# Kernel optimization log

Hardware: AMD Instinct MI355X
Metric: run time of the kernel (lower is better)

## Reference

```python
import jax, jax.numpy as jnp
import numpy as np

PAD = 9  # FNO2d self.padding


def conv1x1(x, w, b):
    # x: [B,Ci,H,W], w: [Co,Ci], b: [Co]  (1x1 Conv2d)
    return jnp.einsum('bixy,oi->boxy', x, w) + b[None, :, None, None]


def setup_inputs() -> dict:
    key = jax.random.key(0)
    ks = jax.random.split(key, 16)
    B, S = 16, 128
    Cin, W, M, D = 5, 64, 16, 4  # raw input channels, width, modes, depth
    scale = 1.0 / (W * W)
    f32 = jnp.float32
    inp = {}
    inp['x'] = jax.random.normal(ks[0], (B, Cin, S, S), dtype=f32)
    # lifting Linear p: in_channel=Cin+2 (grid appended) -> width
    inp['p_w'] = 0.1 * jax.random.normal(ks[1], (Cin + 2, W), dtype=f32)
    inp['p_b'] = jnp.zeros((W,), dtype=f32)
    # spectral weights, stored as real/imag pairs: [D,2,Ci,Co,M,M]
    inp['sw1'] = scale * jax.random.uniform(ks[2], (D, 2, W, W, M, M), dtype=f32)
    inp['sw2'] = scale * jax.random.uniform(ks[3], (D, 2, W, W, M, M), dtype=f32)
    # per-layer MLP (two 1x1 convs) and skip 1x1 conv w
    inp['mlp1_w'] = 0.05 * jax.random.normal(ks[4], (D, W, W), dtype=f32)
    inp['mlp1_b'] = jnp.zeros((D, W), dtype=f32)
    inp['mlp2_w'] = 0.05 * jax.random.normal(ks[5], (D, W, W), dtype=f32)
    inp['mlp2_b'] = jnp.zeros((D, W), dtype=f32)
    inp['ww'] = 0.05 * jax.random.normal(ks[6], (D, W, W), dtype=f32)
    inp['wb'] = jnp.zeros((D, W), dtype=f32)
    # projection MLP q: width -> 4*width -> 1
    inp['q1_w'] = 0.05 * jax.random.normal(ks[7], (4 * W, W), dtype=f32)
    inp['q1_b'] = jnp.zeros((4 * W,), dtype=f32)
    inp['q2_w'] = 0.05 * jax.random.normal(ks[8], (1, 4 * W), dtype=f32)
    inp['q2_b'] = jnp.zeros((1,), dtype=f32)
    return inp


def reference(x, p_w, p_b, sw1, sw2, mlp1_w, mlp1_b, mlp2_w, mlp2_b, ww, wb, q1_w, q1_b, q2_w, q2_b):
    B, _, Sx, Sy = x.shape
    D, _, _, Co, M, _ = sw1.shape
    # grid channels (x, y) in [0,1]
    gx = jnp.broadcast_to(jnp.linspace(0.0, 1.0, Sx, dtype=x.dtype)[None, None, :, None], (B, 1, Sx, Sy))
    gy = jnp.broadcast_to(jnp.linspace(0.0, 1.0, Sy, dtype=x.dtype)[None, None, None, :], (B, 1, Sx, Sy))
    x = jnp.concatenate([x, gx, gy], axis=1)
    # lifting (Linear over channel dim)
    x = jnp.einsum('bcxy,cd->bdxy', x, p_w) + p_b[None, :, None, None]
    # pad bottom/right
    x = jnp.pad(x, ((0, 0), (0, 0), (0, PAD), (0, PAD)))
    H, Wd = x.shape[-2], x.shape[-1]
    for i in range(D):
        # spectral conv: rfft2 -> low-mode complex mult -> irfft2
        xf = jnp.fft.rfft2(x)  # [B,C,H,Wd//2+1] complex64
        w1 = sw1[i, 0] + 1j * sw1[i, 1]
        w2 = sw2[i, 0] + 1j * sw2[i, 1]
        top = jnp.einsum('bixy,ioxy->boxy', xf[:, :, :M, :M], w1)
        bot = jnp.einsum('bixy,ioxy->boxy', xf[:, :, H - M:, :M], w2)
        of = jnp.zeros((B, Co, H, Wd // 2 + 1), dtype=xf.dtype)
        of = of.at[:, :, :M, :M].set(top).at[:, :, H - M:, :M].set(bot)
        x1 = jnp.fft.irfft2(of, s=(H, Wd))
        # MLP on spectral branch
        x1 = conv1x1(x1, mlp1_w[i], mlp1_b[i])
        x1 = jax.nn.gelu(x1, approximate=False)
        x1 = conv1x1(x1, mlp2_w[i], mlp2_b[i])
        # skip 1x1 conv
        x2 = conv1x1(x, ww[i], wb[i])
        x = jax.nn.gelu(x1 + x2, approximate=False)
    # crop padding, project
    x = x[..., :H - PAD, :Wd - PAD]
    x = conv1x1(x, q1_w, q1_b)
    x = jax.nn.gelu(x, approximate=False)
    x = conv1x1(x, q2_w, q2_b)
    return x
```

## Files before the change

### kernel.cpp

```cpp
#include <hip/hip_runtime.h>
#include <math.h>

#define BB 16
#define CH 64
#define SS 128
#define HH 137
#define XS 144
#define CS (137 * 144)
#define MM 16
#define KK 32
#define NL 4

__device__ __forceinline__ float gelu_f(float x) {
    return 0.5f * x * (1.0f + erff(x * 0.70710678118654752440f));
}

__global__ void k_init(float2* __restrict__ Wy, float2* __restrict__ Wx,
                       float2* __restrict__ WyT, float* __restrict__ wcomb,
                       const float* __restrict__ m2w, const float* __restrict__ wwp) {
    int t = blockIdx.x * 256 + threadIdx.x;
    const double PI2 = 6.283185307179586476925286766559;
    if (t < 2192) {
        int y = t >> 4, k = t & 15;
        int m = (y * k) % HH;
        double ang = -PI2 * (double)m / (double)HH;
        Wy[t] = make_float2((float)cos(ang), (float)sin(ang));
    } else if (t < 6576) {
        int u = t - 2192;
        int x = u >> 5, ki = u & 31;
        int K = (ki < 16) ? ki : (105 + ki);
        int m = (x * K) % HH;
        double ang = -PI2 * (double)m / (double)HH;
        Wx[u] = make_float2((float)cos(ang), (float)sin(ang));
    } else if (t < 8768) {
        int u = t - 6576;
        int ky = u / 137, y = u - ky * 137;
        int m = (y * ky) % HH;
        double ang = -PI2 * (double)m / (double)HH;
        WyT[u] = make_float2((float)cos(ang), (float)sin(ang));
    } else if (t < 41536) {
        int u = t - 8768;
        int layer = u >> 13;
        int r = u & 8191;
        int i = r >> 7, c = r & 127;
        float v;
        if (c < 64) v = m2w[layer * 4096 + c * 64 + i];
        else        v = wwp[layer * 4096 + (c - 64) * 64 + i];
        wcomb[u] = v;
    }
}

__global__ void k_wtrans(const float* __restrict__ sw1, const float* __restrict__ sw2,
                         int layer, float* __restrict__ WS) {
    int d = blockIdx.x * 256 + threadIdx.x;
    int reim = d & 1;
    int o  = (d >> 1) & 63;
    int i  = (d >> 7) & 63;
    int ky = (d >> 13) & 15;
    int kx = (d >> 17) & 31;
    const float* src = (kx < 16) ? sw1 : sw2;
    int kk = kx & 15;
    WS[d] = src[layer * 2097152 + reim * 1048576 + i * 16384 + o * 256 + kk * 16 + ky];
}

__global__ void k_proj(const float* __restrict__ x, const float* __restrict__ pw,
                       const float* __restrict__ pb, float* __restrict__ X0) {
    int t = blockIdx.x * 256 + threadIdx.x;
    int b = t / (CH * CS);
    int r = t - b * (CH * CS);
    int d = r / CS;
    int s = r - d * CS;
    int X = s / XS, Y = s - X * XS;
    float v = 0.f;
    if (X < SS && Y < SS) {
        v = pb[d];
        #pragma unroll
        for (int c = 0; c < 5; c++)
            v += x[((b * 5 + c) * SS + X) * SS + Y] * pw[c * CH + d];
        v += ((float)X * (1.0f / 127.0f)) * pw[5 * CH + d];
        v += ((float)Y * (1.0f / 127.0f)) * pw[6 * CH + d];
    }
    X0[t] = v;
}

__global__ void __launch_bounds__(256) k_dfty3(const float* __restrict__ X0,
                                               const float2* __restrict__ Wy,
                                               float* __restrict__ Tf) {
    __shared__ float sXT[32 * 260];
    __shared__ float sWy[HH * 32];
    int tid = threadIdx.x;
    int r0b = blockIdx.x * 256;
    int bi0 = r0b / 137;
    int xx0 = r0b - bi0 * 137;
    for (int idx = tid; idx < HH * MM; idx += 256) {
        float2 w = Wy[idx];
        sWy[idx * 2] = w.x;
        sWy[idx * 2 + 1] = w.y;
    }
    int rowg = tid >> 2, kg = tid & 3;
    int r0 = rowg * 4, k0 = kg * 8;
    float acc[4][8];
    #pragma unroll
    for (int a = 0; a < 4; a++)
        #pragma unroll
        for (int c = 0; c < 8; c++) acc[a][c] = 0.f;
    for (int yc = 0; yc < 5; yc++) {
        int y0c = yc * 32;
        int ylen = (y0c + 32 <= HH) ? 32 : (HH - y0c);
        __syncthreads();
        for (int k = 0; k < 8; k++) {
            int idx = k * 256 + tid;
            int r = idx >> 3, q = idx & 7;
            int xx = xx0 + r, bi = bi0;
            if (xx >= 137) { xx -= 137; bi++; }
            if (xx >= 137) { xx -= 137; bi++; }
            int y = y0c + 4 * q;
            size_t off = (size_t)bi * CS + xx * XS + y;
            float4 v;
            if (y + 4 <= HH) {
                v = *(const float4*)&X0[off];
            } else {
                v.x = (y     < HH) ? X0[off]     : 0.f;
                v.y = (y + 1 < HH) ? X0[off + 1] : 0.f;
                v.z = (y + 2 < HH) ? X0[off + 2] : 0.f;
                v.w = (y + 3 < HH) ? X0[off + 3] : 0.f;
            }
            int yy = 4 * q;
            sXT[(yy    ) * 260 + r] = v.x;
            sXT[(yy + 1) * 260 + r] = v.y;
            sXT[(yy + 2) * 260 + r] = v.z;
            sXT[(yy + 3) * 260 + r] = v.w;
        }
        __syncthreads();
        for (int yy = 0; yy < ylen; yy++) {
            int y = y0c + yy;
            float4 wA = *(const float4*)&sWy[y * 32 + k0];
            float4 wB = *(const float4*)&sWy[y * 32 + k0 + 4];
            float4 v  = *(const float4*)&sXT[yy * 260 + r0];
            float wv[8] = {wA.x, wA.y, wA.z, wA.w, wB.x, wB.y, wB.z, wB.w};
            float vv[4] = {v.x, v.y, v.z, v.w};
            #pragma unroll
            for (int a = 0; a < 4; a++)
                #pragma unroll
                for (int c = 0; c < 8; c++) acc[a][c] += vv[a] * wv[c];
        }
    }
    #pragma unroll
    for (int a = 0; a < 4; a++) {
        size_t rb = (size_t)(r0b + r0 + a) * 32 + k0;
        *(float4*)&Tf[rb]     = make_float4(acc[a][0], acc[a][1], acc[a][2], acc[a][3]);
        *(float4*)&Tf[rb + 4] = make_float4(acc[a][4], acc[a][5], acc[a][6], acc[a][7]);
    }
}

__global__ void __launch_bounds__(512) k_dftx2(const float* __restrict__ Tf,
                                               const float2* __restrict__ Wx,
                                               float2* __restrict__ F) {
    __shared__ float sT[HH * 32];
    __shared__ float2 sWx[HH * 32];
    int tid = threadIdx.x;
    int bi = blockIdx.x;
    const float4* tg = (const float4*)(Tf + (size_t)bi * (HH * 32));
    for (int idx = tid; idx < HH * 8; idx += 512) ((float4*)sT)[idx] = tg[idx];
    const float4* wg = (const float4*)Wx;
    for (int idx = tid; idx < HH * 16; idx += 512) ((float4*)sWx)[idx] = wg[idx];
    __syncthreads();
    int ky = tid & 15, kx = tid >> 4;
    float fr = 0.f, fi = 0.f;
    const float2* sT2 = (const float2*)sT;
    #pragma unroll 4
    for (int x = 0; x < HH; x++) {
        float2 t = sT2[x * 16 + ky];
        float2 w = sWx[x * 32 + kx];
        fr += t.x * w.x - t.y * w.y;
        fi += t.x * w.y + t.y * w.x;
    }
    F[(size_t)bi * 512 + tid] = make_float2(fr, fi);
}

__global__ void __launch_bounds__(256) k_specmul2(const float2* __restrict__ F,
                                                  const float2* __restrict__ WS,
                                                  float2* __restrict__ G) {
    int tid = threadIdx.x;
    int o = tid & 63;
    int kyq = __builtin_amdgcn_readfirstlane(tid >> 6);
    int kx = blockIdx.x;
    int bg = blockIdx.y;
    for (int bq = 0; bq < 2; bq++) {
        int b = bg * 2 + bq;
        float gr[4], gi[4];
        #pragma unroll
        for (int j = 0; j < 4; j++) { gr[j] = 0.f; gi[j] = 0.f; }
        for (int i = 0; i < CH; i++) {
            const float2* Fb = F + ((size_t)(b * CH + i) * KK + kx) * MM + kyq * 4;
            const float2* Wb = WS + ((size_t)(kx * MM + kyq * 4) * CH + i) * CH + o;
            #pragma unroll
            for (int j = 0; j < 4; j++) {
                float2 f = Fb[j];
                float2 w = Wb[(size_t)j * CH * CH];
                gr[j] += f.x * w.x - f.y * w.y;
                gi[j] += f.x * w.y + f.y * w.x;
            }
        }
        float* Gf = (float*)G;
        size_t base = (((size_t)(b * CH + o) * KK + kx) * MM + kyq * 4) * 2;
        *(float4*)&Gf[base]     = make_float4(gr[0], gi[0], gr[1], gi[1]);
        *(float4*)&Gf[base + 4] = make_float4(gr[2], gi[2], gr[3], gi[3]);
    }
}

__global__ void __launch_bounds__(128) k_mlp1m(const float* __restrict__ Gf,
                                               const float* __restrict__ m1w, int layer,
                                               float* __restrict__ G2f) {
    __shared__ float sG[64 * 64];
    __shared__ float sM[64 * 68];
    int tid = threadIdx.x;
    int b = blockIdx.y;
    int c0b = blockIdx.x * 64;
    for (int idx = tid; idx < 4096; idx += 128) {
        int o = idx >> 6, c = idx & 63;
        sG[idx] = Gf[(size_t)(b * CH + o) * 1024 + c0b + c];
    }
    for (int idx = tid; idx < 4096; idx += 128) {
        int p = idx >> 6, o = idx & 63;
        sM[o * 68 + p] = m1w[layer * 4096 + p * 64 + o];
    }
    __syncthreads();
    int cg = tid & 15, pg = tid >> 4;
    int c0 = cg * 4, p0 = pg * 8;
    float acc[8][4];
    #pragma unroll
    for (int a = 0; a < 8; a++)
        #pragma unroll
        for (int c = 0; c < 4; c++) acc[a][c] = 0.f;
    for (int o = 0; o < CH; o++) {
        float4 wA = *(const float4*)&sM[o * 68 + p0];
        float4 wB = *(const float4*)&sM[o * 68 + p0 + 4];
        float4 v  = *(const float4*)&sG[o * 64 + c0];
        float wv[8] = {wA.x, wA.y, wA.z, wA.w, wB.x, wB.y, wB.z, wB.w};
        float vv[4] = {v.x, v.y, v.z, v.w};
        #pragma unroll
        for (int a = 0; a < 8; a++)
            #pragma unroll
            for (int c = 0; c < 4; c++) acc[a][c] += wv[a] * vv[c];
    }
    #pragma unroll
    for (int a = 0; a < 8; a++)
        *(float4*)&G2f[(size_t)(b * CH + p0 + a) * 1024 + c0b + c0] =
            make_float4(acc[a][0], acc[a][1], acc[a][2], acc[a][3]);
}

__global__ void __launch_bounds__(256) k_invx2(const float2* __restrict__ G2,
                                               const float2* __restrict__ Wx,
                                               float2* __restrict__ Hh) {
    __shared__ float2 sG[512];
    __shared__ float2 sWx[HH * 32];
    int tid = threadIdx.x;
    int bo = blockIdx.x;
    const float4* gg = (const float4*)(G2 + (size_t)bo * 512);
    if (tid < 256) ((float4*)sG)[tid] = gg[tid];
    const float4* wg = (const float4*)Wx;
    for (int idx = tid; idx < HH * 16; idx += 256) ((float4*)sWx)[idx] = wg[idx];
    __syncthreads();
    for (int it = 0; it < 9; it++) {
        int item = it * 256 + tid;
        if (item >= HH * 16) break;
        int x = item >> 4, ky = item & 15;
        float hr = 0.f, hi = 0.f;
        #pragma unroll 4
        for (int kx = 0; kx < KK; kx++) {
            float2 g = sG[kx * 16 + ky];
            float2 w = sWx[x * 32 + kx];
            hr += g.x * w.x + g.y * w.y;
            hi += g.y * w.x - g.x * w.y;
        }
        float sc = (ky == 0 ? 1.0f : 2.0f) / 18769.0f;
        Hh[(size_t)bo * (HH * 16) + item] = make_float2(hr * sc, hi * sc);
    }
}

__global__ void __launch_bounds__(192) k_fuse(float* __restrict__ X0,
    const float2* __restrict__ Hh, const float2* __restrict__ WyT,
    const float* __restrict__ wcomb, const float* __restrict__ m1b,
    const float* __restrict__ m2b, const float* __restrict__ wb, int layer) {
    int tid = threadIdx.x;
    int x = blockIdx.x;
    int b = blockIdx.y;
    int yy = (tid < HH) ? tid : (HH - 1);
    float wr[16], wi[16];
    #pragma unroll
    for (int ky = 0; ky < 16; ky++) {
        float2 w = WyT[ky * HH + yy];
        wr[ky] = w.x; wi[ky] = w.y;
    }
    float acc[64];
    #pragma unroll
    for (int o = 0; o < 64; o++) acc[o] = 0.f;
    const float* wl = wcomb + layer * 8192;
    for (int i = 0; i < CH; i++) {
        const float4* h4 = (const float4*)(Hh + ((size_t)(b * CH + i) * HH + x) * 16);
        float x1 = m1b[layer * CH + i];
        #pragma unroll
        for (int j = 0; j < 8; j++) {
            float4 a = h4[j];
            x1 += a.x * wr[2 * j] + a.y * wi[2 * j] + a.z * wr[2 * j + 1] + a.w * wi[2 * j + 1];
        }
        x1 = gelu_f(x1);
        float x0 = X0[(size_t)(b * CH + i) * CS + x * XS + yy];
        const float4* wc = (const float4*)(wl + i * 128);
        #pragma unroll
        for (int oq = 0; oq < 16; oq++) {
            float4 wa = wc[oq];
            float4 wsk = wc[16 + oq];
            acc[4 * oq + 0] += wa.x * x1 + wsk.x * x0;
            acc[4 * oq + 1] += wa.y * x1 + wsk.y * x0;
            acc[4 * oq + 2] += wa.z * x1 + wsk.z * x0;
            acc[4 * oq + 3] += wa.w * x1 + wsk.w * x0;
        }
    }
    bool act = (tid < HH);
    #pragma unroll
    for (int o = 0; o < 64; o++) {
        float bias = m2b[layer * CH + o] + wb[layer * CH + o];
        float r = gelu_f(acc[o] + bias);
        if (act) X0[(size_t)(b * CH + o) * CS + x * XS + tid] = r;
    }
}

__global__ void __launch_bounds__(256) k_final5(const float* __restrict__ X0,
    const float* __restrict__ q1w, const float* __restrict__ q1b,
    const float* __restrict__ q2w, const float* __restrict__ q2b,
    float* __restrict__ out) {
    __shared__ float sV[CH * 132];
    __shared__ float sW[CH * 68];
    int tid = threadIdx.x;
    int b = blockIdx.y;
    int X = blockIdx.x;
    for (int k = 0; k < 8; k++) {
        int idx = k * 256 + tid;
        int i = idx >> 5, yq = idx & 31;
        *(float4*)&sV[i * 132 + yq * 4] =
            *(const float4*)&X0[(size_t)(b * CH + i) * CS + X * XS + yq * 4];
    }
    int hg = tid & 15, yg = tid >> 4;
    int h0 = hg * 4, y0 = yg * 8;
    float qacc[8];
    #pragma unroll
    for (int c = 0; c < 8; c++) qacc[c] = 0.f;
    for (int hc = 0; hc < 4; hc++) {
        __syncthreads();
        for (int idx = tid; idx < 4096; idx += 256) {
            int h = idx >> 6, i = idx & 63;
            sW[i * 68 + h] = q1w[(hc * 64 + h) * 64 + i];
        }
        __syncthreads();
        float acc[4][8];
        #pragma unroll
        for (int a = 0; a < 4; a++)
            #pragma unroll
            for (int c = 0; c < 8; c++) acc[a][c] = 0.f;
        for (int i = 0; i < CH; i++) {
            float4 w  = *(const float4*)&sW[i * 68 + h0];
            float4 vA = *(const float4*)&sV[i * 132 + y0];
            float4 vB = *(const float4*)&sV[i * 132 + y0 + 4];
            float wv[4] = {w.x, w.y, w.z, w.w};
            float vv[8] = {vA.x, vA.y, vA.z, vA.w, vB.x, vB.y, vB.z, vB.w};
            #pragma unroll
            for (int a = 0; a < 4; a++)
                #pragma unroll
                for (int c = 0; c < 8; c++) acc[a][c] += wv[a] * vv[c];
        }
        #pragma unroll
        for (int a = 0; a < 4; a++) {
            int h = hc * 64 + h0 + a;
            float qb = q1b[h], q2v = q2w[h];
            #pragma unroll
            for (int c = 0; c < 8; c++)
                qacc[c] += q2v * gelu_f(acc[a][c] + qb);
        }
    }
    __syncthreads();
    float* sRed = sW;
    *(float4*)&sRed[hg * 132 + y0]     = make_float4(qacc[0], qacc[1], qacc[2], qacc[3]);
    *(float4*)&sRed[hg * 132 + y0 + 4] = make_float4(qacc[4], qacc[5], qacc[6], qacc[7]);
    __syncthreads();
    if (tid < 128) {
        float r = q2b[0];
        #pragma unroll
        for (int g = 0; g < 16; g++) r += sRed[g * 132 + tid];
        out[(b * SS + X) * SS + tid] = r;
    }
}

extern "C" void kernel_launch(void* const* d_in, const int* in_sizes, int n_in,
                              void* d_out, int out_size, void* d_ws, size_t ws_size,
                              hipStream_t stream) {
    const float* x   = (const float*)d_in[0];
    const float* p_w = (const float*)d_in[1];
    const float* p_b = (const float*)d_in[2];
    const float* sw1 = (const float*)d_in[3];
    const float* sw2 = (const float*)d_in[4];
    const float* m1w = (const float*)d_in[5];
    const float* m1b = (const float*)d_in[6];
    const float* m2w = (const float*)d_in[7];
    const float* m2b = (const float*)d_in[8];
    const float* wwp = (const float*)d_in[9];
    const float* wbp = (const float*)d_in[10];
    const float* q1w = (const float*)d_in[11];
    const float* q1b = (const float*)d_in[12];
    const float* q2w = (const float*)d_in[13];
    const float* q2b = (const float*)d_in[14];

    float* ws = (float*)d_ws;
    float*  X0   = ws;
    float*  Tf   = X0 + (size_t)BB * CH * CS;
    float2* F    = (float2*)(Tf + (size_t)140288 * 32);
    float2* G    = F + (size_t)524288;
    float2* Wy   = G + (size_t)524288;
    float2* Wx   = Wy + 2192;
    float2* WyT  = Wx + 4384;
    float*  wcomb = (float*)(WyT + 2192);
    float*  WS   = wcomb + 32768;

    k_init<<<163, 256, 0, stream>>>(Wy, Wx, WyT, wcomb, m2w, wwp);
    k_proj<<<(BB * CH * CS) / 256, 256, 0, stream>>>(x, p_w, p_b, X0);
    for (int layer = 0; layer < NL; layer++) {
        k_wtrans<<<16384, 256, 0, stream>>>(sw1, sw2, layer, WS);
        k_dfty3<<<548, 256, 0, stream>>>(X0, Wy, Tf);
        k_dftx2<<<1024, 512, 0, stream>>>(Tf, Wx, F);
        k_specmul2<<<dim3(32, 8), 256, 0, stream>>>(F, (const float2*)WS, G);
        k_mlp1m<<<dim3(16, BB), 128, 0, stream>>>((const float*)G, m1w, layer, (float*)F);
        k_invx2<<<1024, 256, 0, stream>>>(F, Wx, (float2*)Tf);
        k_fuse<<<dim3(HH, BB), 192, 0, stream>>>(X0, (const float2*)Tf, WyT, wcomb,
                                                 m1b, m2b, wbp, layer);
    }
    k_final5<<<dim3(SS, BB), 256, 0, stream>>>(X0, q1w, q1b, q2w, q2b, (float*)d_out);
}
```

Before: 1.689 ms.

## Split fused inverse-y DFT and channel mix into register-tiled kernels

Replaces the per-row k_fuse kernel, which held 64 accumulators per thread and streamed weights from global memory, with two kernels. The first does the inverse y-DFT plus the first bias and GELU as a shared-memory register-tiled matmul and writes an intermediate X1 buffer. The second does the combined mlp2 and skip channel mix as another tiled matmul from shared memory. It also shrinks the row stride from 144 to 140 to cut padded traffic. In exchange it adds a full-size intermediate write and read and one extra launch per layer, and WS now aliases the X1 buffer.

```diff
diff --git a/kernel.cpp b/kernel.cpp
--- a/kernel.cpp
+++ b/kernel.cpp
@@ -5,11 +5,12 @@
 #define CH 64
 #define SS 128
 #define HH 137
-#define XS 144
-#define CS (137 * 144)
+#define XS 140
+#define CS (137 * 140)
 #define MM 16
 #define KK 32
 #define NL 4
+#define NROW 140288
 
 __device__ __forceinline__ float gelu_f(float x) {
     return 0.5f * x * (1.0f + erff(x * 0.70710678118654752440f));
@@ -17,6 +18,7 @@
 
 __global__ void k_init(float2* __restrict__ Wy, float2* __restrict__ Wx,
                        float2* __restrict__ WyT, float* __restrict__ wcomb,
+                       float* __restrict__ WTy,
                        const float* __restrict__ m2w, const float* __restrict__ wwp) {
     int t = blockIdx.x * 256 + threadIdx.x;
     const double PI2 = 6.283185307179586476925286766559;
@@ -47,6 +49,17 @@
         if (c < 64) v = m2w[layer * 4096 + c * 64 + i];
         else        v = wwp[layer * 4096 + (c - 64) * 64 + i];
         wcomb[u] = v;
+    } else if (t < 46144) {
+        int u = t - 41536;
+        int f = u / 144, y = u - f * 144;
+        float v = 0.f;
+        if (y < HH) {
+            int ky = f >> 1;
+            int m = (y * ky) % HH;
+            double ang = -PI2 * (double)m / (double)HH;
+            v = (f & 1) ? (float)sin(ang) : (float)cos(ang);
+        }
+        WTy[u] = v;
     }
 }
 
@@ -279,51 +292,126 @@
     }
 }
 
-__global__ void __launch_bounds__(192) k_fuse(float* __restrict__ X0,
-    const float2* __restrict__ Hh, const float2* __restrict__ WyT,
-    const float* __restrict__ wcomb, const float* __restrict__ m1b,
-    const float* __restrict__ m2b, const float* __restrict__ wb, int layer) {
-    int tid = threadIdx.x;
-    int x = blockIdx.x;
+__global__ void __launch_bounds__(256) k_invyg(const float* __restrict__ Hhf,
+                                               const float* __restrict__ WTy,
+                                               const float* __restrict__ m1b, int layer,
+                                               float* __restrict__ X1) {
+    __shared__ float sHT[32 * 60];
+    __shared__ float sW[32 * 144];
+    int tid = threadIdx.x;
+    int row0 = blockIdx.x * 56;
+    for (int idx = tid; idx < 512; idx += 256) {
+        int r = idx >> 3, q = idx & 7;
+        int row = row0 + r;
+        float4 v = make_float4(0.f, 0.f, 0.f, 0.f);
+        if (r < 56 && row < NROW)
+            v = *(const float4*)&Hhf[(size_t)row * 32 + q * 4];
+        sHT[(4 * q + 0) * 60 + r] = v.x;
+        sHT[(4 * q + 1) * 60 + r] = v.y;
+        sHT[(4 * q + 2) * 60 + r] = v.z;
+        sHT[(4 * q + 3) * 60 + r] = v.w;
+    }
+    for (int idx = tid; idx < 1152; idx += 256)
+        ((float4*)sW)[idx] = ((const float4*)WTy)[idx];
+    __syncthreads();
+    if (tid >= 252) return;
+    int rg = tid / 18, cg = tid - rg * 18;
+    int r0 = rg * 4, c0 = cg * 8;
+    float acc[4][8];
+    #pragma unroll
+    for (int a = 0; a < 4; a++)
+        #pragma unroll
+        for (int c = 0; c < 8; c++) acc[a][c] = 0.f;
+    for (int k = 0; k < 32; k++) {
+        float4 rv = *(const float4*)&sHT[k * 60 + r0];
+        float4 wA = *(const float4*)&sW[k * 144 + c0];
+        float4 wB = *(const float4*)&sW[k * 144 + c0 + 4];
+        float rr[4] = {rv.x, rv.y, rv.z, rv.w};
+        float wv[8] = {wA.x, wA.y, wA.z, wA.w, wB.x, wB.y, wB.z, wB.w};
+        #pragma unroll
+        for (int a = 0; a < 4; a++)
+            #pragma unroll
+            for (int c = 0; c < 8; c++) acc[a][c] += rr[a] * wv[c];
+    }
+    #pragma unroll
+    for (int a = 0; a < 4; a++) {
+        int row = row0 + r0 + a;
+        if (row >= NROW) continue;
+        unsigned bo = (unsigned)row / 137u;
+        int x = row - (int)bo * 137;
+        int o = bo & 63;
+        float b1v = m1b[layer * CH + o];
+        float g[8];
+        #pragma unroll
+        for (int c = 0; c < 8; c++) g[c] = gelu_f(acc[a][c] + b1v);
+        size_t base = (size_t)bo * CS + x * XS;
+        if (c0 + 8 <= HH) {
+            *(float4*)&X1[base + c0]     = make_float4(g[0], g[1], g[2], g[3]);
+            *(float4*)&X1[base + c0 + 4] = make_float4(g[4], g[5], g[6], g[7]);
+        } else {
+            #pragma unroll
+            for (int c = 0; c < 8; c++)
+                if (c0 + c < HH) X1[base + c0 + c] = g[c];
+        }
+    }
+}
+
+__global__ void __launch_bounds__(256) k_tail3(float* __restrict__ X0,
+    const float* __restrict__ X1, const float* __restrict__ wcomb,
+    const float* __restrict__ b2, const float* __restrict__ wb, int layer) {
+    __shared__ float sV[CH * 132];
+    __shared__ float sW[CH * 68];
+    int tid = threadIdx.x;
     int b = blockIdx.y;
-    int yy = (tid < HH) ? tid : (HH - 1);
-    float wr[16], wi[16];
-    #pragma unroll
-    for (int ky = 0; ky < 16; ky++) {
-        float2 w = WyT[ky * HH + yy];
-        wr[ky] = w.x; wi[ky] = w.y;
-    }
-    float acc[64];
-    #pragma unroll
-    for (int o = 0; o < 64; o++) acc[o] = 0.f;
+    int s0 = blockIdx.x * 128;
+    int og = tid & 15, pg = tid >> 4;
+    int o0 = og * 4, p0 = pg * 8;
+    float acc[4][8];
+    #pragma unroll
+    for (int a = 0; a < 4; a++)
+        #pragma unroll
+        for (int c = 0; c < 8; c++) acc[a][c] = 0.f;
     const float* wl = wcomb + layer * 8192;
-    for (int i = 0; i < CH; i++) {
-        const float4* h4 = (const float4*)(Hh + ((size_t)(b * CH + i) * HH + x) * 16);
-        float x1 = m1b[layer * CH + i];
-        #pragma unroll
-        for (int j = 0; j < 8; j++) {
-            float4 a = h4[j];
-            x1 += a.x * wr[2 * j] + a.y * wi[2 * j] + a.z * wr[2 * j + 1] + a.w * wi[2 * j + 1];
-        }
-        x1 = gelu_f(x1);
-        float x0 = X0[(size_t)(b * CH + i) * CS + x * XS + yy];
-        const float4* wc = (const float4*)(wl + i * 128);
-        #pragma unroll
-        for (int oq = 0; oq < 16; oq++) {
-            float4 wa = wc[oq];
-            float4 wsk = wc[16 + oq];
-            acc[4 * oq + 0] += wa.x * x1 + wsk.x * x0;
-            acc[4 * oq + 1] += wa.y * x1 + wsk.y * x0;
-            acc[4 * oq + 2] += wa.z * x1 + wsk.z * x0;
-            acc[4 * oq + 3] += wa.w * x1 + wsk.w * x0;
-        }
-    }
-    bool act = (tid < HH);
-    #pragma unroll
-    for (int o = 0; o < 64; o++) {
-        float bias = m2b[layer * CH + o] + wb[layer * CH + o];
-        float r = gelu_f(acc[o] + bias);
-        if (act) X0[(size_t)(b * CH + o) * CS + x * XS + tid] = r;
+
+    #pragma unroll
+    for (int pass = 0; pass < 2; pass++) {
+        const float* src = pass ? X0 : X1;
+        for (int idx = tid; idx < 2048; idx += 256) {
+            int i = idx >> 5, p4 = (idx & 31) * 4;
+            float4 v = make_float4(0.f, 0.f, 0.f, 0.f);
+            int s = s0 + p4;
+            if (s + 4 <= CS) v = *(const float4*)&src[(size_t)(b * CH + i) * CS + s];
+            *(float4*)&sV[i * 132 + p4] = v;
+        }
+        for (int idx = tid; idx < 4096; idx += 256) {
+            int i = idx >> 6, o = idx & 63;
+            sW[i * 68 + o] = wl[i * 128 + (pass ? 64 + o : o)];
+        }
+        __syncthreads();
+        for (int i = 0; i < CH; i++) {
+            float4 w  = *(const float4*)&sW[i * 68 + o0];
+            float4 vA = *(const float4*)&sV[i * 132 + p0];
+            float4 vB = *(const float4*)&sV[i * 132 + p0 + 4];
+            float wv[4] = {w.x, w.y, w.z, w.w};
+            float vv[8] = {vA.x, vA.y, vA.z, vA.w, vB.x, vB.y, vB.z, vB.w};
+            #pragma unroll
+            for (int a = 0; a < 4; a++)
+                #pragma unroll
+                for (int c = 0; c < 8; c++) acc[a][c] += wv[a] * vv[c];
+        }
+        __syncthreads();
+    }
+    #pragma unroll
+    for (int a = 0; a < 4; a++) {
+        float bia = b2[layer * CH + o0 + a] + wb[layer * CH + o0 + a];
+        float g[8];
+        #pragma unroll
+        for (int c = 0; c < 8; c++) g[c] = gelu_f(acc[a][c] + bia);
+        size_t rowb = (size_t)(b * CH + o0 + a) * CS + s0 + p0;
+        if (s0 + p0 + 4 <= CS)
+            *(float4*)&X0[rowb] = make_float4(g[0], g[1], g[2], g[3]);
+        if (s0 + p0 + 8 <= CS)
+            *(float4*)&X0[rowb + 4] = make_float4(g[4], g[5], g[6], g[7]);
     }
 }
 
@@ -413,16 +501,18 @@
 
     float* ws = (float*)d_ws;
     float*  X0   = ws;
-    float*  Tf   = X0 + (size_t)BB * CH * CS;
-    float2* F    = (float2*)(Tf + (size_t)140288 * 32);
+    float*  X1   = X0 + (size_t)BB * CH * CS;
+    float*  WS   = X1;
+    float*  Tf   = X1 + (size_t)BB * CH * CS;
+    float2* F    = (float2*)(Tf + (size_t)NROW * 32);
     float2* G    = F + (size_t)524288;
     float2* Wy   = G + (size_t)524288;
     float2* Wx   = Wy + 2192;
     float2* WyT  = Wx + 4384;
     float*  wcomb = (float*)(WyT + 2192);
-    float*  WS   = wcomb + 32768;
-
-    k_init<<<163, 256, 0, stream>>>(Wy, Wx, WyT, wcomb, m2w, wwp);
+    float*  WTy  = wcomb + 32768;
+
+    k_init<<<181, 256, 0, stream>>>(Wy, Wx, WyT, wcomb, WTy, m2w, wwp);
     k_proj<<<(BB * CH * CS) / 256, 256, 0, stream>>>(x, p_w, p_b, X0);
     for (int layer = 0; layer < NL; layer++) {
         k_wtrans<<<16384, 256, 0, stream>>>(sw1, sw2, layer, WS);
@@ -431,8 +521,8 @@
         k_specmul2<<<dim3(32, 8), 256, 0, stream>>>(F, (const float2*)WS, G);
         k_mlp1m<<<dim3(16, BB), 128, 0, stream>>>((const float*)G, m1w, layer, (float*)F);
         k_invx2<<<1024, 256, 0, stream>>>(F, Wx, (float2*)Tf);
-        k_fuse<<<dim3(HH, BB), 192, 0, stream>>>(X0, (const float2*)Tf, WyT, wcomb,
-                                                 m1b, m2b, wbp, layer);
+        k_invyg<<<(NROW + 55) / 56, 256, 0, stream>>>(Tf, WTy, m1b, layer, X1);
+        k_tail3<<<dim3((CS + 127) / 128, BB), 256, 0, stream>>>(X0, X1, wcomb, m2b, wbp, layer);
     }
     k_final5<<<dim3(SS, BB), 256, 0, stream>>>(X0, q1w, q1b, q2w, q2b, (float*)d_out);
 }
```

Result: no change. 1.717 ms (+1.7%).
